# Kernel optimization log

Hardware: AMD Instinct MI355X
Metric: run time of the kernel (lower is better)

Reference implementation:

```python
import jax, jax.numpy as jnp
import numpy as np

B, T, LD, HD, NH, NL = 8, 16, 256, 512, 8, 6
N = 65           # num_patches + 1 tokens per frame from encoder
AED = 64         # action_embed_dim
NDA = 11         # num_discrete_actions
MLP = 4 * HD


def _ln(x, g, b, eps=1e-5):
    m = jnp.mean(x, -1, keepdims=True)
    v = jnp.mean((x - m) ** 2, -1, keepdims=True)
    return (x - m) / jnp.sqrt(v + eps) * g + b


def setup_inputs() -> dict:
    key = jax.random.key(0)
    ks = iter(jax.random.split(key, 48))
    def nrm(shape):
        return jax.random.normal(next(ks), shape, jnp.float32) * 0.02
    inp = {
        'z_sequence': jax.random.normal(next(ks), (B, T, N, LD), jnp.float32),
        'continuous_actions': jax.random.normal(next(ks), (B, T, 2), jnp.float32),
        'discrete_actions': jax.random.randint(next(ks), (B, T), 0, NDA),
        'w_de': nrm((NDA, AED)),
        'w_cp': nrm((2, AED)), 'b_cp': jnp.zeros((AED,), jnp.float32),
        'w_ap': nrm((2 * AED, HD)), 'b_ap': jnp.zeros((HD,), jnp.float32),
        'w_tp': nrm((LD, HD)), 'b_tp': jnp.zeros((HD,), jnp.float32),
        'w_te': nrm((64, HD)),
        'ln1_g': jnp.ones((NL, HD), jnp.float32), 'ln1_b': jnp.zeros((NL, HD), jnp.float32),
        'wq': nrm((NL, HD, HD)), 'bq': jnp.zeros((NL, HD), jnp.float32),
        'wk': nrm((NL, HD, HD)), 'bk': jnp.zeros((NL, HD), jnp.float32),
        'wv': nrm((NL, HD, HD)), 'bv': jnp.zeros((NL, HD), jnp.float32),
        'wo': nrm((NL, HD, HD)), 'bo': jnp.zeros((NL, HD), jnp.float32),
        'ln2_g': jnp.ones((NL, HD), jnp.float32), 'ln2_b': jnp.zeros((NL, HD), jnp.float32),
        'w1': nrm((NL, HD, MLP)), 'b1': jnp.zeros((NL, MLP), jnp.float32),
        'w2': nrm((NL, MLP, HD)), 'b2': jnp.zeros((NL, HD), jnp.float32),
        'norm_g': jnp.ones((HD,), jnp.float32), 'norm_b': jnp.zeros((HD,), jnp.float32),
        'w_out': nrm((HD, LD)), 'b_out': jnp.zeros((LD,), jnp.float32),
        'residual_weight': jnp.float32(0.5),
    }
    return inp


def reference(z_sequence, continuous_actions, discrete_actions,
              w_de, w_cp, b_cp, w_ap, b_ap, w_tp, b_tp, w_te,
              ln1_g, ln1_b, wq, bq, wk, bk, wv, bv, wo, bo,
              ln2_g, ln2_b, w1, b1, w2, b2,
              norm_g, norm_b, w_out, b_out, residual_weight):
    Bq, Tq, Nq, Dq = z_sequence.shape
    hd = HD // NH
    scale = hd ** -0.5
    # --- per-timestep action + patch token embedding (vectorized over T) ---
    de = w_de[discrete_actions]                          # (B,T,AED)
    ce = continuous_actions @ w_cp + b_cp                # (B,T,AED)
    ac = jnp.concatenate([de, ce], -1)                   # (B,T,2*AED)
    at = (ac @ w_ap + b_ap)[:, :, None, :]               # (B,T,1,HD) action token
    pt = z_sequence @ w_tp + b_tp                        # (B,T,N,HD)
    te = w_te[:Tq][None, :, None, :]                     # (1,T,1,HD) time embedding
    x = jnp.concatenate([at + te, pt + te], axis=2)      # (B,T,1+N,HD) interleaved
    S = Tq * (Nq + 1)
    x = x.reshape(Bq, S, HD)
    # --- block-causal mask: True = cannot attend ---
    ts = jnp.repeat(jnp.arange(Tq), Nq + 1)
    mask = ts[None, :] > ts[:, None]                     # (S,S)

    def body(h, p):
        g1, be1, Wq, Bq_, Wk, Bk_, Wv, Bv_, Wo, Bo_, g2, be2, W1, B1, W2, B2 = p
        y = _ln(h, g1, be1)
        q = (y @ Wq + Bq_).reshape(Bq, S, NH, hd)
        k = (y @ Wk + Bk_).reshape(Bq, S, NH, hd)
        v = (y @ Wv + Bv_).reshape(Bq, S, NH, hd)
        sc = jnp.einsum('bqhd,bkhd->bhqk', q, k) * scale
        sc = jnp.where(mask[None, None], -jnp.inf, sc)
        a = jax.nn.softmax(sc, axis=-1)
        o = jnp.einsum('bhqk,bkhd->bqhd', a, v).reshape(Bq, S, HD)
        h = h + o @ Wo + Bo_
        y = _ln(h, g2, be2)
        h = h + jax.nn.gelu(y @ W1 + B1, approximate=False) @ W2 + B2
        return h, None

    x, _ = jax.lax.scan(body, x, (ln1_g, ln1_b, wq, bq, wk, bk, wv, bv, wo, bo,
                                  ln2_g, ln2_b, w1, b1, w2, b2))
    x = _ln(x, norm_g, norm_b)
    patch_out = x.reshape(Bq, Tq, Nq + 1, HD)[:, :, 1:, :] @ w_out + b_out
    alpha = jax.nn.sigmoid(residual_weight)
    return z_sequence + alpha * patch_out
```

## Files before the change

kernel.cpp:

```cpp
#include <hip/hip_runtime.h>
#include <hip/hip_bf16.h>
#include <cmath>

typedef __attribute__((ext_vector_type(8)))  __bf16 bf16x8;
typedef __attribute__((ext_vector_type(4)))  float  f32x4;
typedef __attribute__((ext_vector_type(16))) float  f32x16;
typedef const __attribute__((address_space(1))) void* as1cv;
typedef __attribute__((address_space(3))) void*       as3v;

static constexpr int BB = 8, TT = 16, NN = 65, LD = 256, HD = 512, NH = 8, NL = 6;
static constexpr int SS    = TT * (NN + 1);
static constexpr int ROWS  = BB * SS;
static constexpr int PROWS = BB * TT * NN;
static constexpr int MLPD  = 2048;

__global__ void transpose_cast(const float* __restrict__ in, __bf16* __restrict__ out,
                               int R, int C, size_t ibs, size_t obs)
{
  __shared__ float t[32][33];
  in  += ibs * blockIdx.z;
  out += obs * blockIdx.z;
  int bx = blockIdx.x * 32, by = blockIdx.y * 32;
  #pragma unroll
  for (int i = threadIdx.y; i < 32; i += 8)
    t[i][threadIdx.x] = in[(size_t)(by + i) * C + bx + threadIdx.x];
  __syncthreads();
  #pragma unroll
  for (int i = threadIdx.y; i < 32; i += 8)
    out[(size_t)(bx + i) * R + by + threadIdx.x] = (__bf16)t[threadIdx.x][i];
}

__global__ __launch_bounds__(256) void cast_bf16(const float* __restrict__ in,
                                                 __bf16* __restrict__ out)
{
  int i = (blockIdx.x * 256 + threadIdx.x) * 8;
  float4 a = *(const float4*)(in + i);
  float4 b = *(const float4*)(in + i + 4);
  bf16x8 o;
  o[0]=(__bf16)a.x; o[1]=(__bf16)a.y; o[2]=(__bf16)a.z; o[3]=(__bf16)a.w;
  o[4]=(__bf16)b.x; o[5]=(__bf16)b.y; o[6]=(__bf16)b.z; o[7]=(__bf16)b.w;
  *(bf16x8*)(out + i) = o;
}

__global__ void build_bqkv(const float* __restrict__ bq, const float* __restrict__ bk,
                           const float* __restrict__ bv, float* __restrict__ out)
{
  int i = blockIdx.x * 256 + threadIdx.x;
  int L = i / 1536, c = i % 1536;
  float v = (c < 512) ? bq[L*512 + c] : (c < 1024 ? bk[L*512 + c - 512] : bv[L*512 + c - 1024]);
  out[i] = v;
}

template<int FLAGS>
__global__ __launch_bounds__(256)
void gemm_bt(const __bf16* __restrict__ A, const __bf16* __restrict__ Bt,
             const float* __restrict__ bias, const float* __restrict__ resid,
             float* __restrict__ outF, __bf16* __restrict__ outB, __bf16* __restrict__ outB2,
             int M, int N, int K)
{
  __shared__ __bf16 As[128 * 64];
  __shared__ __bf16 Bs[128 * 64];
  const int tid = threadIdx.x;
  const int lane = tid & 63, w = tid >> 6;
  const int g = lane >> 4, cl = lane & 15;
  const int wr = w >> 1, wc = w & 1;
  const int tm = blockIdx.y * 128, tn = blockIdx.x * 128;

  f32x4 acc[4][4];
  const f32x4 zero4 = {0.f, 0.f, 0.f, 0.f};
  #pragma unroll
  for (int m = 0; m < 4; m++)
    #pragma unroll
    for (int n = 0; n < 4; n++) acc[m][n] = zero4;

  const int nk = K >> 6;
  for (int kt = 0; kt < nk; ++kt) {
    __syncthreads();
    const __bf16* Ag = A  + (size_t)tm * K + kt * 64;
    const __bf16* Bg = Bt + (size_t)tn * K + kt * 64;
    #pragma unroll
    for (int p = 0; p < 4; p++) {
      int c = p * 256 + tid;
      int row = c >> 3, j = c & 7;
      int jj = j ^ (row & 7);
      const __bf16* sa = Ag + (size_t)row * K + jj * 8;
      const __bf16* sb = Bg + (size_t)row * K + jj * 8;
      __bf16* la = &As[(p * 4 + w) * 512];
      __bf16* lb = &Bs[(p * 4 + w) * 512];
      __builtin_amdgcn_global_load_lds((as1cv)sa, (as3v)la, 16, 0, 0);
      __builtin_amdgcn_global_load_lds((as1cv)sb, (as3v)lb, 16, 0, 0);
    }
    __syncthreads();
    #pragma unroll
    for (int kk = 0; kk < 2; kk++) {
      bf16x8 af[4], bfr[4];
      #pragma unroll
      for (int m = 0; m < 4; m++) {
        int row = wr * 64 + m * 16 + cl;
        int j16 = (kk * 4 + g) ^ (row & 7);
        af[m] = *(const bf16x8*)&As[row * 64 + j16 * 8];
      }
      #pragma unroll
      for (int n = 0; n < 4; n++) {
        int row = wc * 64 + n * 16 + cl;
        int j16 = (kk * 4 + g) ^ (row & 7);
        bfr[n] = *(const bf16x8*)&Bs[row * 64 + j16 * 8];
      }
      #pragma unroll
      for (int m = 0; m < 4; m++)
        #pragma unroll
        for (int n = 0; n < 4; n++)
          acc[m][n] = __builtin_amdgcn_mfma_f32_16x16x32_bf16(af[m], bfr[n], acc[m][n], 0, 0, 0);
    }
  }
  float bv[4];
  #pragma unroll
  for (int n = 0; n < 4; n++) bv[n] = bias[tn + wc * 64 + n * 16 + cl];
  #pragma unroll
  for (int m = 0; m < 4; m++) {
    int Rb = tm + wr * 64 + m * 16 + g * 4;
    #pragma unroll
    for (int i = 0; i < 4; i++) {
      int R = Rb + i;
      #pragma unroll
      for (int n = 0; n < 4; n++) {
        int C = tn + wc * 64 + n * 16 + cl;
        float v = acc[m][n][i] + bv[n];
        if (FLAGS & 1) v = 0.5f * v * (1.f + erff(v * 0.70710678118f));
        if (FLAGS & 2) v += resid[(size_t)R * N + C];
        if (FLAGS & 8) outF[(size_t)R * N + C] = v;
        if (FLAGS & 4) outB[(size_t)R * N + C] = (__bf16)v;
        if (FLAGS & 32) {
          if (C < 1024) {
            outB[(size_t)R * 1024 + C] = (__bf16)v;
          } else {
            int bb2 = R / SS, s2 = R % SS;
            int cc = C - 1024, hh = cc >> 6, dd = cc & 63;
            outB2[((size_t)((bb2 * NH + hh) * 64 + dd)) * SS + s2] = (__bf16)v;
          }
        }
      }
    }
  }
}

__global__ __launch_bounds__(256) void ln_bf16(const float* __restrict__ in,
    const float* __restrict__ gam, const float* __restrict__ bet, __bf16* __restrict__ out)
{
  int w = threadIdx.x >> 6, l = threadIdx.x & 63;
  size_t row = (size_t)blockIdx.x * 4 + w;
  const float4* x4 = (const float4*)(in + row * HD);
  float4 v0 = x4[l], v1 = x4[l + 64];
  float s  = v0.x + v0.y + v0.z + v0.w + v1.x + v1.y + v1.z + v1.w;
  float q2 = v0.x*v0.x + v0.y*v0.y + v0.z*v0.z + v0.w*v0.w
           + v1.x*v1.x + v1.y*v1.y + v1.z*v1.z + v1.w*v1.w;
  #pragma unroll
  for (int m = 1; m < 64; m <<= 1) { s += __shfl_xor(s, m); q2 += __shfl_xor(q2, m); }
  float mean = s * (1.f / HD);
  float rstd = rsqrtf(q2 * (1.f / HD) - mean * mean + 1e-5f);
  int c0 = l * 4, c1 = 256 + l * 4;
  float4 g0 = *(const float4*)(gam + c0), g1 = *(const float4*)(gam + c1);
  float4 e0 = *(const float4*)(bet + c0), e1 = *(const float4*)(bet + c1);
  __bf16* o = out + row * HD;
  o[c0+0] = (__bf16)((v0.x-mean)*rstd*g0.x + e0.x);
  o[c0+1] = (__bf16)((v0.y-mean)*rstd*g0.y + e0.y);
  o[c0+2] = (__bf16)((v0.z-mean)*rstd*g0.z + e0.z);
  o[c0+3] = (__bf16)((v0.w-mean)*rstd*g0.w + e0.w);
  o[c1+0] = (__bf16)((v1.x-mean)*rstd*g1.x + e1.x);
  o[c1+1] = (__bf16)((v1.y-mean)*rstd*g1.y + e1.y);
  o[c1+2] = (__bf16)((v1.z-mean)*rstd*g1.z + e1.z);
  o[c1+3] = (__bf16)((v1.w-mean)*rstd*g1.w + e1.w);
}

__global__ __launch_bounds__(64) void act_embed(const float* __restrict__ cont,
    const int* __restrict__ disc, const float* __restrict__ w_de,
    const float* __restrict__ w_cp, const float* __restrict__ b_cp,
    const float* __restrict__ w_ap, const float* __restrict__ b_ap,
    const float* __restrict__ w_te, float* __restrict__ x)
{
  int t = blockIdx.x, b = blockIdx.y, l = threadIdx.x;
  int da = disc[b * TT + t];
  float c0 = cont[(b * TT + t) * 2], c1 = cont[(b * TT + t) * 2 + 1];
  int c = l * 8;
  float accv[8];
  #pragma unroll
  for (int j = 0; j < 8; j++) accv[j] = b_ap[c + j];
  for (int i = 0; i < 64; i++) {
    float ai = w_de[da * 64 + i];
    #pragma unroll
    for (int j = 0; j < 8; j++) accv[j] += ai * w_ap[i * HD + c + j];
  }
  for (int i = 0; i < 64; i++) {
    float ce = c0 * w_cp[i] + c1 * w_cp[64 + i] + b_cp[i];
    #pragma unroll
    for (int j = 0; j < 8; j++) accv[j] += ce * w_ap[(64 + i) * HD + c + j];
  }
  #pragma unroll
  for (int j = 0; j < 8; j++)
    x[((size_t)(b * SS) + t * 66) * HD + c + j] = accv[j] + w_te[t * HD + c + j];
}

__global__ __launch_bounds__(256) void assemble_patch(const float* __restrict__ pt,
    const float* __restrict__ te, float* __restrict__ x)
{
  int idx = (blockIdx.x * 256 + threadIdx.x) * 4;
  int c = idx & (HD - 1);
  int r = idx >> 9;
  int n = r % NN; int bt = r / NN; int t = bt & (TT - 1); int bb = bt >> 4;
  float4 v  = *(const float4*)(pt + idx);
  float4 tv = *(const float4*)(te + t * HD + c);
  v.x += tv.x; v.y += tv.y; v.z += tv.z; v.w += tv.w;
  *(float4*)(x + ((size_t)(bb * SS + t * 66 + 1 + n)) * HD + c) = v;
}

__device__ inline unsigned pkbf(float lo, float hi2) {
  unsigned short a = __builtin_bit_cast(unsigned short, (__bf16)lo);
  unsigned short b = __builtin_bit_cast(unsigned short, (__bf16)hi2);
  return (unsigned)a | ((unsigned)b << 16);
}

__global__ __launch_bounds__(256) void attn_fwd(const __bf16* __restrict__ qk,
    const __bf16* __restrict__ vT, __bf16* __restrict__ o)
{
  const int w = threadIdx.x >> 6, lane = threadIdx.x & 63;
  const int h = blockIdx.y, b = blockIdx.z;
  int qt;
  if (blockIdx.x == 8) qt = (w == 0) ? 16 : -1;
  else {
    int j = blockIdx.x;
    qt = (w == 0) ? j : (w == 1) ? 32 - j : (w == 2) ? 8 + j : 24 - j;
  }
  __shared__ float red[4][32];
  if (qt < 0) return;
  const int l31 = lane & 31, hi = lane >> 5;
  const int q = qt * 32 + l31;
  const int kend = (q / 66 + 1) * 66;
  const int nkv = (((qt * 32 + 31) / 66 + 1) * 66 + 31) >> 5;

  bf16x8 qf[4];
  const __bf16* qbase = qk + (size_t)(b * SS + q) * 1024 + h * 64 + hi * 8;
  #pragma unroll
  for (int s = 0; s < 4; s++) qf[s] = *(const bf16x8*)(qbase + s * 16);

  const f32x16 z16 = {0,0,0,0,0,0,0,0,0,0,0,0,0,0,0,0};
  f32x16 accA = z16, accB = z16;
  float m = -1e30f, lsum = 0.f;

  for (int kb = 0; kb < nkv; kb++) {
    const int K0 = kb * 32;
    const __bf16* kbase = qk + (size_t)(b * SS + K0 + l31) * 1024 + 512 + h * 64 + hi * 8;
    bf16x8 kf0 = *(const bf16x8*)(kbase);
    bf16x8 kf1 = *(const bf16x8*)(kbase + 16);
    bf16x8 kf2 = *(const bf16x8*)(kbase + 32);
    bf16x8 kf3 = *(const bf16x8*)(kbase + 48);
    const __bf16* vbase = vT + (size_t)((b * NH + h) * 64 + l31) * SS + K0 + hi * 8;
    bf16x8 vf00 = *(const bf16x8*)(vbase);
    bf16x8 vf10 = *(const bf16x8*)(vbase + 16);
    bf16x8 vf01 = *(const bf16x8*)(vbase + (size_t)32 * SS);
    bf16x8 vf11 = *(const bf16x8*)(vbase + (size_t)32 * SS + 16);

    f32x16 st = z16;
    st = __builtin_amdgcn_mfma_f32_32x32x16_bf16(kf0, qf[0], st, 0, 0, 0);
    st = __builtin_amdgcn_mfma_f32_32x32x16_bf16(kf1, qf[1], st, 0, 0, 0);
    st = __builtin_amdgcn_mfma_f32_32x32x16_bf16(kf2, qf[2], st, 0, 0, 0);
    st = __builtin_amdgcn_mfma_f32_32x32x16_bf16(kf3, qf[3], st, 0, 0, 0);

    float p[16];
    #pragma unroll
    for (int r = 0; r < 16; r++) {
      int kg = K0 + (r & 3) + 8 * (r >> 2) + 4 * hi;
      p[r] = (kg < kend) ? st[r] * 0.125f : -1e30f;
    }
    float mx = fmaxf(fmaxf(fmaxf(p[0],p[1]),fmaxf(p[2],p[3])),
                     fmaxf(fmaxf(p[4],p[5]),fmaxf(p[6],p[7])));
    mx = fmaxf(mx, fmaxf(fmaxf(fmaxf(p[8],p[9]),fmaxf(p[10],p[11])),
                         fmaxf(fmaxf(p[12],p[13]),fmaxf(p[14],p[15]))));
    mx = fmaxf(mx, __shfl_xor(mx, 32));
    if (__any(mx > m + 8.f)) {
      float nm = fmaxf(m, mx);
      float alp = __expf(m - nm);
      m = nm; lsum *= alp;
      if (lane < 32) red[w][lane] = alp;
      asm volatile("s_waitcnt lgkmcnt(0)" ::: "memory");
      float4 a0 = *(const float4*)&red[w][hi * 4];
      float4 a1 = *(const float4*)&red[w][hi * 4 + 8];
      float4 a2 = *(const float4*)&red[w][hi * 4 + 16];
      float4 a3 = *(const float4*)&red[w][hi * 4 + 24];
      float afv[16] = {a0.x,a0.y,a0.z,a0.w, a1.x,a1.y,a1.z,a1.w,
                       a2.x,a2.y,a2.z,a2.w, a3.x,a3.y,a3.z,a3.w};
      #pragma unroll
      for (int r = 0; r < 16; r++) { accA[r] *= afv[r]; accB[r] *= afv[r]; }
    }
    float rs;
    #pragma unroll
    for (int r = 0; r < 16; r++) p[r] = __expf(p[r] - m);
    rs = ((p[0]+p[1])+(p[2]+p[3])) + ((p[4]+p[5])+(p[6]+p[7]))
       + ((p[8]+p[9])+(p[10]+p[11])) + ((p[12]+p[13])+(p[14]+p[15]));
    rs += __shfl_xor(rs, 32);
    lsum += rs;
    unsigned a0p = pkbf(p[0], p[1]),  a1p = pkbf(p[2], p[3]);
    unsigned a2p = pkbf(p[4], p[5]),  a3p = pkbf(p[6], p[7]);
    unsigned b0p = pkbf(p[8], p[9]),  b1p = pkbf(p[10], p[11]);
    unsigned b2p = pkbf(p[12], p[13]), b3p = pkbf(p[14], p[15]);
    unsigned s0 = __shfl_xor(a0p, 32), s1 = __shfl_xor(a1p, 32);
    unsigned s2 = __shfl_xor(a2p, 32), s3 = __shfl_xor(a3p, 32);
    unsigned t0 = __shfl_xor(b0p, 32), t1 = __shfl_xor(b1p, 32);
    unsigned t2 = __shfl_xor(b2p, 32), t3 = __shfl_xor(b3p, 32);
    union { unsigned u[4]; bf16x8 v; } af0, af1;
    af0.u[0] = hi ? s2 : a0p;  af0.u[1] = hi ? s3 : a1p;
    af0.u[2] = hi ? a2p : s0;  af0.u[3] = hi ? a3p : s1;
    af1.u[0] = hi ? t2 : b0p;  af1.u[1] = hi ? t3 : b1p;
    af1.u[2] = hi ? b2p : t0;  af1.u[3] = hi ? b3p : t1;
    accA = __builtin_amdgcn_mfma_f32_32x32x16_bf16(af0.v, vf00, accA, 0, 0, 0);
    accA = __builtin_amdgcn_mfma_f32_32x32x16_bf16(af1.v, vf10, accA, 0, 0, 0);
    accB = __builtin_amdgcn_mfma_f32_32x32x16_bf16(af0.v, vf01, accB, 0, 0, 0);
    accB = __builtin_amdgcn_mfma_f32_32x32x16_bf16(af1.v, vf11, accB, 0, 0, 0);
  }
  if (lane < 32) red[w][lane] = 1.f / lsum;
  asm volatile("s_waitcnt lgkmcnt(0)" ::: "memory");
  float4 i0 = *(const float4*)&red[w][hi * 4];
  float4 i1 = *(const float4*)&red[w][hi * 4 + 8];
  float4 i2 = *(const float4*)&red[w][hi * 4 + 16];
  float4 i3 = *(const float4*)&red[w][hi * 4 + 24];
  float iv[16] = {i0.x,i0.y,i0.z,i0.w, i1.x,i1.y,i1.z,i1.w,
                  i2.x,i2.y,i2.z,i2.w, i3.x,i3.y,i3.z,i3.w};
  __bf16* obase = o + (size_t)(b * SS + qt * 32) * HD + h * 64 + l31;
  #pragma unroll
  for (int r = 0; r < 16; r++) {
    int qrow = (r & 3) + 8 * (r >> 2) + 4 * hi;
    obase[(size_t)qrow * HD]      = (__bf16)(accA[r] * iv[r]);
    obase[(size_t)qrow * HD + 32] = (__bf16)(accB[r] * iv[r]);
  }
}

__global__ __launch_bounds__(256) void final_add(const float* __restrict__ z,
    const float* __restrict__ po, const float* __restrict__ rw, float* __restrict__ out)
{
  int idx = (blockIdx.x * 256 + threadIdx.x) * 4;
  int ld = idx & (LD - 1);
  int r = idx >> 8;
  int n = r % NN; int bt = r / NN; int t = bt & (TT - 1); int bb = bt >> 4;
  float alpha = 1.f / (1.f + __expf(-rw[0]));
  float4 zv = *(const float4*)(z + idx);
  float4 pv = *(const float4*)(po + ((size_t)(bb * SS + t * 66 + 1 + n)) * LD + ld);
  float4 ov;
  ov.x = zv.x + alpha * pv.x; ov.y = zv.y + alpha * pv.y;
  ov.z = zv.z + alpha * pv.z; ov.w = zv.w + alpha * pv.w;
  *(float4*)(out + idx) = ov;
}

extern "C" void kernel_launch(void* const* d_in, const int* in_sizes, int n_in,
                              void* d_out, int out_size, void* d_ws, size_t ws_size,
                              hipStream_t stream)
{
  const float* z    = (const float*)d_in[0];
  const float* cont = (const float*)d_in[1];
  const int*   disc = (const int*)d_in[2];
  const float* w_de = (const float*)d_in[3];
  const float* w_cp = (const float*)d_in[4];
  const float* b_cp = (const float*)d_in[5];
  const float* w_ap = (const float*)d_in[6];
  const float* b_ap = (const float*)d_in[7];
  const float* w_tp = (const float*)d_in[8];
  const float* b_tp = (const float*)d_in[9];
  const float* w_te = (const float*)d_in[10];
  const float* ln1g = (const float*)d_in[11];
  const float* ln1b = (const float*)d_in[12];
  const float* wq   = (const float*)d_in[13];
  const float* bq   = (const float*)d_in[14];
  const float* wk   = (const float*)d_in[15];
  const float* bk   = (const float*)d_in[16];
  const float* wv   = (const float*)d_in[17];
  const float* bv   = (const float*)d_in[18];
  const float* wo   = (const float*)d_in[19];
  const float* bo   = (const float*)d_in[20];
  const float* ln2g = (const float*)d_in[21];
  const float* ln2b = (const float*)d_in[22];
  const float* w1   = (const float*)d_in[23];
  const float* b1   = (const float*)d_in[24];
  const float* w2   = (const float*)d_in[25];
  const float* b2   = (const float*)d_in[26];
  const float* nog  = (const float*)d_in[27];
  const float* nob  = (const float*)d_in[28];
  const float* wout = (const float*)d_in[29];
  const float* bout = (const float*)d_in[30];
  const float* rw   = (const float*)d_in[31];
  float* out = (float*)d_out;

  char* p = (char*)d_ws;
  auto alloc = [&](size_t bytes) -> char* {
    char* r = p; p += (bytes + 255) & ~(size_t)255; return r;
  };
  __bf16* wqkvt = (__bf16*)alloc((size_t)NL * 1536 * 512 * 2);
  __bf16* wot_  = (__bf16*)alloc((size_t)NL * 512 * 512 * 2);
  __bf16* w1t   = (__bf16*)alloc((size_t)NL * 512 * 2048 * 2);
  __bf16* w2t   = (__bf16*)alloc((size_t)NL * 512 * 2048 * 2);
  __bf16* wtpt  = (__bf16*)alloc((size_t)512 * 256 * 2);
  __bf16* woutt = (__bf16*)alloc((size_t)256 * 512 * 2);
  float*  bqkv  = (float*)alloc((size_t)NL * 1536 * 4);
  __bf16* zbf   = (__bf16*)alloc((size_t)PROWS * LD * 2);
  float*  x     = (float*)alloc((size_t)ROWS * HD * 4);
  __bf16* y     = (__bf16*)alloc((size_t)ROWS * HD * 2);
  __bf16* qkb   = (__bf16*)alloc((size_t)ROWS * 1024 * 2);
  __bf16* vtb   = (__bf16*)alloc((size_t)ROWS * HD * 2);
  __bf16* ob    = (__bf16*)alloc((size_t)ROWS * HD * 2);
  __bf16* mid   = (__bf16*)alloc((size_t)ROWS * MLPD * 2);
  float*  ptb   = (float*)alloc((size_t)PROWS * HD * 4);
  (void)in_sizes; (void)n_in; (void)out_size; (void)ws_size;

  dim3 tb(32, 8);
  transpose_cast<<<dim3(16, 16, 6), tb, 0, stream>>>(wq, wqkvt,          512,  512,  262144, 786432);
  transpose_cast<<<dim3(16, 16, 6), tb, 0, stream>>>(wk, wqkvt + 262144, 512,  512,  262144, 786432);
  transpose_cast<<<dim3(16, 16, 6), tb, 0, stream>>>(wv, wqkvt + 524288, 512,  512,  262144, 786432);
  transpose_cast<<<dim3(16, 16, 6), tb, 0, stream>>>(wo, wot_,           512,  512,  262144, 262144);
  transpose_cast<<<dim3(64, 16, 6), tb, 0, stream>>>(w1, w1t,            512,  2048, 1048576, 1048576);
  transpose_cast<<<dim3(16, 64, 6), tb, 0, stream>>>(w2, w2t,            2048, 512,  1048576, 1048576);
  transpose_cast<<<dim3(16, 8, 1),  tb, 0, stream>>>(w_tp, wtpt,         256,  512,  0, 0);
  transpose_cast<<<dim3(8, 16, 1),  tb, 0, stream>>>(wout, woutt,        512,  256,  0, 0);
  build_bqkv<<<36, 256, 0, stream>>>(bq, bk, bv, bqkv);
  cast_bf16<<<(PROWS * LD) / 2048, 256, 0, stream>>>(z, zbf);

  gemm_bt<8><<<dim3(4, 65), 256, 0, stream>>>(zbf, wtpt, b_tp, nullptr, ptb, nullptr, nullptr,
                                              PROWS, 512, 256);
  act_embed<<<dim3(16, 8), 64, 0, stream>>>(cont, disc, w_de, w_cp, b_cp, w_ap, b_ap, w_te, x);
  assemble_patch<<<(PROWS * HD) / 1024, 256, 0, stream>>>(ptb, w_te, x);

  for (int L = 0; L < NL; ++L) {
    ln_bf16<<<ROWS / 4, 256, 0, stream>>>(x, ln1g + L*HD, ln1b + L*HD, y);
    gemm_bt<32><<<dim3(12, 66), 256, 0, stream>>>(y, wqkvt + (size_t)L*786432, bqkv + L*1536,
                                                  nullptr, nullptr, qkb, vtb, ROWS, 1536, 512);
    attn_fwd<<<dim3(9, NH, BB), 256, 0, stream>>>(qkb, vtb, ob);
    gemm_bt<10><<<dim3(4, 66), 256, 0, stream>>>(ob, wot_ + (size_t)L*262144, bo + L*HD,
                                                 x, x, nullptr, nullptr, ROWS, 512, 512);
    ln_bf16<<<ROWS / 4, 256, 0, stream>>>(x, ln2g + L*HD, ln2b + L*HD, y);
    gemm_bt<5><<<dim3(16, 66), 256, 0, stream>>>(y, w1t + (size_t)L*1048576, b1 + L*MLPD,
                                                 nullptr, nullptr, mid, nullptr, ROWS, 2048, 512);
    gemm_bt<10><<<dim3(4, 66), 256, 0, stream>>>(mid, w2t + (size_t)L*1048576, b2 + L*HD,
                                                 x, x, nullptr, nullptr, ROWS, 512, 2048);
  }
  ln_bf16<<<ROWS / 4, 256, 0, stream>>>(x, nog, nob, y);
  gemm_bt<8><<<dim3(2, 66), 256, 0, stream>>>(y, woutt, bout, nullptr, ptb, nullptr, nullptr,
                                              ROWS, 256, 512);
  final_add<<<(PROWS * LD) / 1024, 256, 0, stream>>>(z, ptb, rw, out);
}
```

Measured before the change: 1.284 ms.

## Shrink GEMM tiles, add XCD-aware tile remap, flatten attention grid

Reduces the M tile of the main GEMM from 128 to 64 rows and adds a 64x64 GEMM variant for the narrow N=512/256 projections, so each launch has more workgroups across the MI355X's compute units. Tile indices are remapped so consecutive tiles land on the same XCD, aiming for better L2 reuse of shared operand panels. The attention launch becomes a 1D grid with a similar XCD-grouped mapping of (batch, head, q-block). In exchange, smaller tiles lower arithmetic intensity per workgroup and add global/LDS traffic per FLOP.

```diff
diff --git a/kernel.cpp b/kernel.cpp
--- a/kernel.cpp
+++ b/kernel.cpp
@@ -58,18 +58,23 @@
              float* __restrict__ outF, __bf16* __restrict__ outB, __bf16* __restrict__ outB2,
              int M, int N, int K)
 {
-  __shared__ __bf16 As[128 * 64];
+  __shared__ __bf16 As[64 * 64];
   __shared__ __bf16 Bs[128 * 64];
   const int tid = threadIdx.x;
   const int lane = tid & 63, w = tid >> 6;
   const int g = lane >> 4, cl = lane & 15;
   const int wr = w >> 1, wc = w & 1;
-  const int tm = blockIdx.y * 128, tn = blockIdx.x * 128;
-
-  f32x4 acc[4][4];
+  const int gx = gridDim.x, nwg = gx * gridDim.y;
+  const int orig = blockIdx.y * gx + blockIdx.x;
+  const int q8 = nwg >> 3, r8 = nwg & 7;
+  const int xcd = orig & 7, off = orig >> 3;
+  const int tile = (xcd < r8 ? xcd * (q8 + 1) : r8 * (q8 + 1) + (xcd - r8) * q8) + off;
+  const int tm = (tile / gx) * 64, tn = (tile % gx) * 128;
+
+  f32x4 acc[2][4];
   const f32x4 zero4 = {0.f, 0.f, 0.f, 0.f};
   #pragma unroll
-  for (int m = 0; m < 4; m++)
+  for (int m = 0; m < 2; m++)
     #pragma unroll
     for (int n = 0; n < 4; n++) acc[m][n] = zero4;
 
@@ -79,35 +84,37 @@
     const __bf16* Ag = A  + (size_t)tm * K + kt * 64;
     const __bf16* Bg = Bt + (size_t)tn * K + kt * 64;
     #pragma unroll
+    for (int p = 0; p < 2; p++) {
+      int c = p * 256 + tid;
+      int row = c >> 3, j = c & 7;
+      int jj = j ^ (row & 7);
+      const __bf16* sa = Ag + (size_t)row * K + jj * 8;
+      __builtin_amdgcn_global_load_lds((as1cv)sa, (as3v)&As[(p * 4 + w) * 512], 16, 0, 0);
+    }
+    #pragma unroll
     for (int p = 0; p < 4; p++) {
       int c = p * 256 + tid;
       int row = c >> 3, j = c & 7;
       int jj = j ^ (row & 7);
-      const __bf16* sa = Ag + (size_t)row * K + jj * 8;
       const __bf16* sb = Bg + (size_t)row * K + jj * 8;
-      __bf16* la = &As[(p * 4 + w) * 512];
-      __bf16* lb = &Bs[(p * 4 + w) * 512];
-      __builtin_amdgcn_global_load_lds((as1cv)sa, (as3v)la, 16, 0, 0);
-      __builtin_amdgcn_global_load_lds((as1cv)sb, (as3v)lb, 16, 0, 0);
+      __builtin_amdgcn_global_load_lds((as1cv)sb, (as3v)&Bs[(p * 4 + w) * 512], 16, 0, 0);
     }
     __syncthreads();
     #pragma unroll
     for (int kk = 0; kk < 2; kk++) {
-      bf16x8 af[4], bfr[4];
-      #pragma unroll
-      for (int m = 0; m < 4; m++) {
-        int row = wr * 64 + m * 16 + cl;
-        int j16 = (kk * 4 + g) ^ (row & 7);
-        af[m] = *(const bf16x8*)&As[row * 64 + j16 * 8];
+      bf16x8 af[2], bfr[4];
+      #pragma unroll
+      for (int m = 0; m < 2; m++) {
+        int row = wr * 32 + m * 16 + cl;
+        af[m] = *(const bf16x8*)&As[row * 64 + ((kk * 4 + g) ^ (row & 7)) * 8];
       }
       #pragma unroll
       for (int n = 0; n < 4; n++) {
         int row = wc * 64 + n * 16 + cl;
-        int j16 = (kk * 4 + g) ^ (row & 7);
-        bfr[n] = *(const bf16x8*)&Bs[row * 64 + j16 * 8];
+        bfr[n] = *(const bf16x8*)&Bs[row * 64 + ((kk * 4 + g) ^ (row & 7)) * 8];
       }
       #pragma unroll
-      for (int m = 0; m < 4; m++)
+      for (int m = 0; m < 2; m++)
         #pragma unroll
         for (int n = 0; n < 4; n++)
           acc[m][n] = __builtin_amdgcn_mfma_f32_16x16x32_bf16(af[m], bfr[n], acc[m][n], 0, 0, 0);
@@ -117,8 +124,8 @@
   #pragma unroll
   for (int n = 0; n < 4; n++) bv[n] = bias[tn + wc * 64 + n * 16 + cl];
   #pragma unroll
-  for (int m = 0; m < 4; m++) {
-    int Rb = tm + wr * 64 + m * 16 + g * 4;
+  for (int m = 0; m < 2; m++) {
+    int Rb = tm + wr * 32 + m * 16 + g * 4;
     #pragma unroll
     for (int i = 0; i < 4; i++) {
       int R = Rb + i;
@@ -144,6 +151,91 @@
   }
 }
 
+template<int FLAGS>
+__global__ __launch_bounds__(256)
+void gemm_n64(const __bf16* __restrict__ A, const __bf16* __restrict__ Bt,
+              const float* __restrict__ bias, const float* __restrict__ resid,
+              float* __restrict__ outF, __bf16* __restrict__ outB,
+              int M, int N, int K)
+{
+  __shared__ __bf16 As[64 * 64];
+  __shared__ __bf16 Bs[64 * 64];
+  const int tid = threadIdx.x;
+  const int lane = tid & 63, w = tid >> 6;
+  const int g = lane >> 4, cl = lane & 15;
+  const int wr = w >> 1, wc = w & 1;
+  const int gx = gridDim.x, nwg = gx * gridDim.y;
+  const int orig = blockIdx.y * gx + blockIdx.x;
+  const int q8 = nwg >> 3, r8 = nwg & 7;
+  const int xcd = orig & 7, off = orig >> 3;
+  const int tile = (xcd < r8 ? xcd * (q8 + 1) : r8 * (q8 + 1) + (xcd - r8) * q8) + off;
+  const int tm = (tile / gx) * 64, tn = (tile % gx) * 64;
+
+  f32x4 acc[2][2];
+  const f32x4 zero4 = {0.f, 0.f, 0.f, 0.f};
+  #pragma unroll
+  for (int m = 0; m < 2; m++)
+    #pragma unroll
+    for (int n = 0; n < 2; n++) acc[m][n] = zero4;
+
+  const int nk = K >> 6;
+  for (int kt = 0; kt < nk; ++kt) {
+    __syncthreads();
+    const __bf16* Ag = A  + (size_t)tm * K + kt * 64;
+    const __bf16* Bg = Bt + (size_t)tn * K + kt * 64;
+    #pragma unroll
+    for (int p = 0; p < 2; p++) {
+      int c = p * 256 + tid;
+      int row = c >> 3, j = c & 7;
+      int jj = j ^ (row & 7);
+      const __bf16* sa = Ag + (size_t)row * K + jj * 8;
+      const __bf16* sb = Bg + (size_t)row * K + jj * 8;
+      __builtin_amdgcn_global_load_lds((as1cv)sa, (as3v)&As[(p * 4 + w) * 512], 16, 0, 0);
+      __builtin_amdgcn_global_load_lds((as1cv)sb, (as3v)&Bs[(p * 4 + w) * 512], 16, 0, 0);
+    }
+    __syncthreads();
+    #pragma unroll
+    for (int kk = 0; kk < 2; kk++) {
+      bf16x8 af[2], bfr[2];
+      #pragma unroll
+      for (int m = 0; m < 2; m++) {
+        int row = wr * 32 + m * 16 + cl;
+        af[m] = *(const bf16x8*)&As[row * 64 + ((kk * 4 + g) ^ (row & 7)) * 8];
+      }
+      #pragma unroll
+      for (int n = 0; n < 2; n++) {
+        int row = wc * 32 + n * 16 + cl;
+        bfr[n] = *(const bf16x8*)&Bs[row * 64 + ((kk * 4 + g) ^ (row & 7)) * 8];
+      }
+      #pragma unroll
+      for (int m = 0; m < 2; m++)
+        #pragma unroll
+        for (int n = 0; n < 2; n++)
+          acc[m][n] = __builtin_amdgcn_mfma_f32_16x16x32_bf16(af[m], bfr[n], acc[m][n], 0, 0, 0);
+    }
+  }
+  float bv[2];
+  #pragma unroll
+  for (int n = 0; n < 2; n++) bv[n] = bias[tn + wc * 32 + n * 16 + cl];
+  #pragma unroll
+  for (int m = 0; m < 2; m++) {
+    int Rb = tm + wr * 32 + m * 16 + g * 4;
+    #pragma unroll
+    for (int i = 0; i < 4; i++) {
+      int R = Rb + i;
+      #pragma unroll
+      for (int n = 0; n < 2; n++) {
+        int C = tn + wc * 32 + n * 16 + cl;
+        float v = acc[m][n][i] + bv[n];
+        if (FLAGS & 1) v = 0.5f * v * (1.f + erff(v * 0.70710678118f));
+        if (FLAGS & 2) v += resid[(size_t)R * N + C];
+        if (FLAGS & 8) outF[(size_t)R * N + C] = v;
+        if (FLAGS & 4) outB[(size_t)R * N + C] = (__bf16)v;
+      }
+    }
+  }
+}
+
 __global__ __launch_bounds__(256) void ln_bf16(const float* __restrict__ in,
     const float* __restrict__ gam, const float* __restrict__ bet, __bf16* __restrict__ out)
 {
@@ -223,13 +315,13 @@
     const __bf16* __restrict__ vT, __bf16* __restrict__ o)
 {
   const int w = threadIdx.x >> 6, lane = threadIdx.x & 63;
-  const int h = blockIdx.y, b = blockIdx.z;
+  const int lin = (blockIdx.x & 7) * 72 + (blockIdx.x >> 3);
+  const int b   = lin / 72;
+  const int rem = lin % 72;
+  const int h = rem / 9, j = rem % 9;
   int qt;
-  if (blockIdx.x == 8) qt = (w == 0) ? 16 : -1;
-  else {
-    int j = blockIdx.x;
-    qt = (w == 0) ? j : (w == 1) ? 32 - j : (w == 2) ? 8 + j : 24 - j;
-  }
+  if (j == 8) qt = (w == 0) ? 16 : -1;
+  else        qt = (w == 0) ? j : (w == 1) ? 32 - j : (w == 2) ? 8 + j : 24 - j;
   __shared__ float red[4][32];
   if (qt < 0) return;
   const int l31 = lane & 31, hi = lane >> 5;
@@ -420,26 +512,28 @@
   build_bqkv<<<36, 256, 0, stream>>>(bq, bk, bv, bqkv);
   cast_bf16<<<(PROWS * LD) / 2048, 256, 0, stream>>>(z, zbf);
 
-  gemm_bt<8><<<dim3(4, 65), 256, 0, stream>>>(zbf, wtpt, b_tp, nullptr, ptb, nullptr, nullptr,
-                                              PROWS, 512, 256);
+  gemm_n64<8><<<dim3(8, PROWS / 64), 256, 0, stream>>>(zbf, wtpt, b_tp, nullptr, ptb, nullptr,
+                                                       PROWS, 512, 256);
   act_embed<<<dim3(16, 8), 64, 0, stream>>>(cont, disc, w_de, w_cp, b_cp, w_ap, b_ap, w_te, x);
   assemble_patch<<<(PROWS * HD) / 1024, 256, 0, stream>>>(ptb, w_te, x);
 
   for (int L = 0; L < NL; ++L) {
     ln_bf16<<<ROWS / 4, 256, 0, stream>>>(x, ln1g + L*HD, ln1b + L*HD, y);
-    gemm_bt<32><<<dim3(12, 66), 256, 0, stream>>>(y, wqkvt + (size_t)L*786432, bqkv + L*1536,
-                                                  nullptr, nullptr, qkb, vtb, ROWS, 1536, 512);
-    attn_fwd<<<dim3(9, NH, BB), 256, 0, stream>>>(qkb, vtb, ob);
-    gemm_bt<10><<<dim3(4, 66), 256, 0, stream>>>(ob, wot_ + (size_t)L*262144, bo + L*HD,
-                                                 x, x, nullptr, nullptr, ROWS, 512, 512);
+    gemm_bt<32><<<dim3(12, ROWS / 64), 256, 0, stream>>>(y, wqkvt + (size_t)L*786432,
+                                                         bqkv + L*1536, nullptr, nullptr,
+                                                         qkb, vtb, ROWS, 1536, 512);
+    attn_fwd<<<576, 256, 0, stream>>>(qkb, vtb, ob);
+    gemm_n64<10><<<dim3(8, ROWS / 64), 256, 0, stream>>>(ob, wot_ + (size_t)L*262144, bo + L*HD,
+                                                         x, x, nullptr, ROWS, 512, 512);
     ln_bf16<<<ROWS / 4, 256, 0, stream>>>(x, ln2g + L*HD, ln2b + L*HD, y);
-    gemm_bt<5><<<dim3(16, 66), 256, 0, stream>>>(y, w1t + (size_t)L*1048576, b1 + L*MLPD,
-                                                 nullptr, nullptr, mid, nullptr, ROWS, 2048, 512);
-    gemm_bt<10><<<dim3(4, 66), 256, 0, stream>>>(mid, w2t + (size_t)L*1048576, b2 + L*HD,
-                                                 x, x, nullptr, nullptr, ROWS, 512, 2048);
+    gemm_bt<5><<<dim3(16, ROWS / 64), 256, 0, stream>>>(y, w1t + (size_t)L*1048576, b1 + L*MLPD,
+                                                        nullptr, nullptr, mid, nullptr,
+                                                        ROWS, 2048, 512);
+    gemm_n64<10><<<dim3(8, ROWS / 64), 256, 0, stream>>>(mid, w2t + (size_t)L*1048576, b2 + L*HD,
+                                                         x, x, nullptr, ROWS, 512, 2048);
   }
   ln_bf16<<<ROWS / 4, 256, 0, stream>>>(x, nog, nob, y);
-  gemm_bt<8><<<dim3(2, 66), 256, 0, stream>>>(y, woutt, bout, nullptr, ptb, nullptr, nullptr,
-                                              ROWS, 256, 512);
+  gemm_n64<8><<<dim3(4, ROWS / 64), 256, 0, stream>>>(y, woutt, bout, nullptr, ptb, nullptr,
+                                                      ROWS, 256, 512);
   final_add<<<(PROWS * LD) / 1024, 256, 0, stream>>>(z, ptb, rw, out);
 }
```

Measured after the change: 1.068 ms. -16.8%, faster.
